# Kernel tuning notes

Hardware: AMD Instinct MI355X
Metric: run time of the kernel (lower is better)

## Reference

```python
import jax, jax.numpy as jnp
import numpy as np

B, N = 32, 2048

def _gather(pts, idx):
    # pts: [B,N,C], idx: [B,...] int -> [B,...,C]
    b = pts.shape[0]
    flat = jnp.take_along_axis(pts, idx.reshape(b, -1)[:, :, None], axis=1)
    return flat.reshape(idx.shape + (pts.shape[-1],))

def _fps(xyz, npoint):
    # iterative farthest point sampling, start at index 0
    b, n, _ = xyz.shape
    def step(carry, _):
        dist, far = carry
        centroid = _gather(xyz, far[:, None])            # [B,1,3]
        d = jnp.sum((xyz - centroid) ** 2, axis=-1)      # [B,N]
        dist = jnp.minimum(dist, d)
        nxt = jnp.argmax(dist, axis=-1).astype(jnp.int32)
        return (dist, nxt), far
    init = (jnp.full((b, n), 1e10, xyz.dtype), jnp.zeros((b,), jnp.int32))
    _, idxs = jax.lax.scan(step, init, None, length=npoint)
    return jnp.transpose(idxs)                           # [B,npoint]

def _ball_query(radius, nsample, xyz, new_xyz):
    n = xyz.shape[1]
    sqr = jnp.sum((new_xyz[:, :, None, :] - xyz[:, None, :, :]) ** 2, axis=-1)  # [B,S,N]
    idx = jnp.broadcast_to(jnp.arange(n, dtype=jnp.int32), sqr.shape)
    idx = jnp.where(sqr > radius * radius, n, idx)
    idx = jnp.sort(idx, axis=-1)[:, :, :nsample]
    first = idx[:, :, :1]
    return jnp.where(idx == n, first, idx)               # [B,S,K]

def _mlp_max(x, params):
    # shared per-point MLP (1x1 conv) + max-pool over neighbors (BN at init == identity)
    for W, b in params:
        x = jax.nn.relu(jnp.einsum('bskc,dc->bskd', x, W) + b)
    return jnp.max(x, axis=2)                            # [B,S,out]

def _sa(xyz, points, npoint, radius, nsample, params):
    fidx = _fps(xyz, npoint)
    new_xyz = _gather(xyz, fidx)                         # [B,S,3]
    gidx = _ball_query(radius, nsample, xyz, new_xyz)
    grouped = _gather(xyz, gidx) - new_xyz[:, :, None, :]
    if points is not None:
        grouped = jnp.concatenate([grouped, _gather(points, gidx)], axis=-1)
    return new_xyz, _mlp_max(grouped, params)

def _sa_all(xyz, points, params):
    grouped = jnp.concatenate([xyz, points], axis=-1)[:, None]  # [B,1,N,C+3]
    return _mlp_max(grouped, params)[:, 0]               # [B,out]

def _linear(x, W, b):
    return x @ W.T + b

def _forward(points, grasp_pose, init_pose, final_pose, surfaces,
             sa1_w0, sa1_b0, sa1_w1, sa1_b1, sa1_w2, sa1_b2,
             sa2_w0, sa2_b0, sa2_w1, sa2_b1, sa2_w2, sa2_b2,
             emb_init, emb_final,
             pe_w0, pe_b0, pe_w1, pe_b1, pe_w2, pe_b2,
             fu_w0, fu_b0, fu_w1, fu_b1,
             os_w, os_b, oc_w, oc_b):
    sa1 = [(sa1_w0, sa1_b0), (sa1_w1, sa1_b1), (sa1_w2, sa1_b2)]
    sa2 = [(sa2_w0, sa2_b0), (sa2_w1, sa2_b1), (sa2_w2, sa2_b2)]
    l1_xyz, l1_points = _sa(points, None, 512, 0.2, 32, sa1)
    obj_feat = _sa_all(l1_xyz, l1_points, sa2)           # [B,256]
    ie = emb_init[surfaces[:, 0]]
    fe = emb_final[surfaces[:, 1]]
    x = jnp.concatenate([grasp_pose, init_pose, final_pose, ie, fe], axis=1)
    h = jax.nn.relu(_linear(x, pe_w0, pe_b0))
    h = jax.nn.relu(_linear(h, pe_w1, pe_b1))
    pose_feat = jax.nn.relu(_linear(h, pe_w2, pe_b2))
    fused = jnp.concatenate([obj_feat, pose_feat], axis=1)
    h = jax.nn.relu(_linear(fused, fu_w0, fu_b0))
    hidden = jax.nn.relu(_linear(h, fu_w1, fu_b1))
    return _linear(hidden, os_w, os_b), _linear(hidden, oc_w, oc_b)

def setup_inputs():
    key = jax.random.key(0)
    ks = jax.random.split(key, 24)
    def lin(k, o, i):
        return jax.random.normal(k, (o, i), jnp.float32) * (2.0 / i) ** 0.5
    z = lambda o: jnp.zeros((o,), jnp.float32)
    return {
        'points': jax.random.normal(ks[0], (B, N, 3), jnp.float32),
        'grasp_pose': jax.random.normal(ks[1], (B, 7), jnp.float32),
        'init_pose': jax.random.normal(ks[2], (B, 7), jnp.float32),
        'final_pose': jax.random.normal(ks[3], (B, 7), jnp.float32),
        'surfaces': jax.random.randint(ks[4], (B, 2), 0, 6),
        'sa1_w0': lin(ks[5], 64, 3), 'sa1_b0': z(64),
        'sa1_w1': lin(ks[6], 64, 64), 'sa1_b1': z(64),
        'sa1_w2': lin(ks[7], 128, 64), 'sa1_b2': z(128),
        'sa2_w0': lin(ks[8], 128, 131), 'sa2_b0': z(128),
        'sa2_w1': lin(ks[9], 128, 128), 'sa2_b1': z(128),
        'sa2_w2': lin(ks[10], 256, 128), 'sa2_b2': z(256),
        'emb_init': jax.random.normal(ks[11], (6, 8), jnp.float32),
        'emb_final': jax.random.normal(ks[12], (6, 8), jnp.float32),
        'pe_w0': lin(ks[13], 64, 37), 'pe_b0': z(64),
        'pe_w1': lin(ks[14], 128, 64), 'pe_b1': z(128),
        'pe_w2': lin(ks[15], 128, 128), 'pe_b2': z(128),
        'fu_w0': lin(ks[16], 128, 384), 'fu_b0': z(128),
        'fu_w1': lin(ks[17], 64, 128), 'fu_b1': z(64),
        'os_w': lin(ks[18], 1, 64), 'os_b': z(1),
        'oc_w': lin(ks[19], 1, 64), 'oc_b': z(1),
    }

def reference(points, grasp_pose, init_pose, final_pose, surfaces,
              sa1_w0, sa1_b0, sa1_w1, sa1_b1, sa1_w2, sa1_b2,
              sa2_w0, sa2_b0, sa2_w1, sa2_b1, sa2_w2, sa2_b2,
              emb_init, emb_final,
              pe_w0, pe_b0, pe_w1, pe_b1, pe_w2, pe_b2,
              fu_w0, fu_b0, fu_w1, fu_b1,
              os_w, os_b, oc_w, oc_b):
    return _forward(points, grasp_pose, init_pose, final_pose, surfaces,
                    sa1_w0, sa1_b0, sa1_w1, sa1_b1, sa1_w2, sa1_b2,
                    sa2_w0, sa2_b0, sa2_w1, sa2_b1, sa2_w2, sa2_b2,
                    emb_init, emb_final,
                    pe_w0, pe_b0, pe_w1, pe_b1, pe_w2, pe_b2,
                    fu_w0, fu_b0, fu_w1, fu_b1,
                    os_w, os_b, oc_w, oc_b)
```

## Files before the change

### kernel.cpp

```cpp
#include <hip/hip_runtime.h>

#define DEVINL __device__ __forceinline__

DEVINL float sq3(float ax, float ay, float az, float bx, float by, float bz) {
  float dx = __fsub_rn(ax, bx), dy = __fsub_rn(ay, by), dz = __fsub_rn(az, bz);
  return __fadd_rn(__fadd_rn(__fmul_rn(dx, dx), __fmul_rn(dy, dy)), __fmul_rn(dz, dz));
}

DEVINL float rdlane(float v, int l) {
  return __int_as_float(__builtin_amdgcn_readlane(__float_as_int(v), l));
}

template <int CTRL>
DEVINL float dpp_maxf(float v) {
  int o = __builtin_amdgcn_update_dpp(__float_as_int(v), __float_as_int(v),
                                      CTRL, 0xf, 0xf, false);
  return fmaxf(v, __int_as_float(o));
}
DEVINL float red32_maxf(float v) {
  v = dpp_maxf<0x111>(v); v = dpp_maxf<0x112>(v); v = dpp_maxf<0x114>(v);
  v = dpp_maxf<0x118>(v); v = dpp_maxf<0x142>(v);
  return v;
}
DEVINL float red64_maxf(float v) {
  v = red32_maxf(v); v = dpp_maxf<0x143>(v);
  return v;
}
template <int CTRL>
DEVINL unsigned long long dpp_maxk(unsigned long long k) {
  const unsigned lo = (unsigned)k, hi = (unsigned)(k >> 32);
  const unsigned olo = (unsigned)__builtin_amdgcn_update_dpp(
      (int)lo, (int)lo, CTRL, 0xf, 0xf, false);
  const unsigned ohi = (unsigned)__builtin_amdgcn_update_dpp(
      (int)hi, (int)hi, CTRL, 0xf, 0xf, false);
  const unsigned long long ok = ((unsigned long long)ohi << 32) | olo;
  return (ok > k) ? ok : k;
}
DEVINL unsigned long long red64_maxk(unsigned long long k) {
  k = dpp_maxk<0x111>(k); k = dpp_maxk<0x112>(k); k = dpp_maxk<0x114>(k);
  k = dpp_maxk<0x118>(k); k = dpp_maxk<0x142>(k); k = dpp_maxk<0x143>(k);
  return k;
}

__global__ __launch_bounds__(256) void k_wt(const float* __restrict__ w1,
                                            const float* __restrict__ w2,
                                            float* __restrict__ w1T,
                                            float* __restrict__ w2T) {
  const int i = blockIdx.x * 256 + threadIdx.x;
  if (i < 4096) {
    const int d = i >> 6, c = i & 63;
    w1T[c * 64 + d] = w1[i];
  }
  if (i < 8192) {
    const int e = i >> 6, c = i & 63;
    w2T[c * 128 + e] = w2[i];
  }
}

__global__ __launch_bounds__(256) void k_fps(const float* __restrict__ xyz,
                                             int* __restrict__ fidx) {
  const int b = blockIdx.x, t = threadIdx.x;
  __shared__ float xs[2048], ys[2048], zs[2048];
  __shared__ unsigned long long skey[2][4];
  __shared__ float4 scoord[2][4];
  const float* P = xyz + (size_t)b * 6144;
  for (int i = t; i < 2048; i += 256) {
    xs[i] = P[3 * i]; ys[i] = P[3 * i + 1]; zs[i] = P[3 * i + 2];
  }
  __syncthreads();
  float px[8], py[8], pz[8], dist[8];
#pragma unroll
  for (int j = 0; j < 8; ++j) {
    const int idx = j * 256 + t;
    px[j] = xs[idx]; py[j] = ys[idx]; pz[j] = zs[idx];
    dist[j] = 1e10f;
  }
  int far = 0;
  float cx = xs[0], cy = ys[0], cz = zs[0];
  int* out = fidx + b * 512;
  for (int it = 0; it < 512; ++it) {
    if (t == 0) out[it] = far;
    float bv = -1.0f;
    int bi = 0;
#pragma unroll
    for (int j = 0; j < 8; ++j) {
      const float d = sq3(px[j], py[j], pz[j], cx, cy, cz);
      const float nd = fminf(dist[j], d);
      dist[j] = nd;
      if (nd > bv) { bv = nd; bi = j * 256 + t; }
    }
    unsigned long long key =
        ((unsigned long long)__float_as_uint(bv) << 32) | (unsigned)(2047 - bi);
    key = red64_maxk(key);
    const int par = it & 1;
    if ((t & 63) == 63) {
      const int widx = 2047 - (int)((unsigned)key & 2047u);
      skey[par][t >> 6] = key;
      scoord[par][t >> 6] = make_float4(xs[widx], ys[widx], zs[widx], 0.0f);
    }
    __syncthreads();
    unsigned long long k0 = skey[par][0], k1 = skey[par][1];
    unsigned long long k2 = skey[par][2], k3 = skey[par][3];
    float4 c0 = scoord[par][0], c1 = scoord[par][1];
    float4 c2 = scoord[par][2], c3 = scoord[par][3];
    if (k1 > k0) { k0 = k1; c0 = c1; }
    if (k3 > k2) { k2 = k3; c2 = c3; }
    if (k2 > k0) { k0 = k2; c0 = c2; }
    far = 2047 - (int)((unsigned)k0 & 2047u);
    cx = c0.x; cy = c0.y; cz = c0.z;
  }
}

__global__ __launch_bounds__(256) void k_ballq(const float* __restrict__ xyz,
                                               const int* __restrict__ fidx,
                                               float* __restrict__ new_xyz,
                                               int* __restrict__ gidx,
                                               int* __restrict__ gn) {
  const int gw = (blockIdx.x * 256 + threadIdx.x) >> 6;
  const int lane = threadIdx.x & 63;
  const int b = gw >> 9;
  const float* P = xyz + (size_t)b * 6144;
  const int cidx = fidx[gw];
  const float cx = P[3 * cidx], cy = P[3 * cidx + 1], cz = P[3 * cidx + 2];
  if (lane < 3) new_xyz[(size_t)gw * 3 + lane] = P[3 * cidx + lane];
  int* g = gidx + (size_t)gw * 32;
  int base = 0;
  for (int c0 = 0; c0 < 2048; c0 += 64) {
    const int idx = c0 + lane;
    const float d = sq3(cx, cy, cz, P[3 * idx], P[3 * idx + 1], P[3 * idx + 2]);
    const bool in = !(d > 0.04f);
    const unsigned long long m = __ballot(in);
    if (in) {
      const int pos = base + (int)__popcll(m & ((1ull << lane) - 1ull));
      if (pos < 32) g[pos] = idx;
    }
    base += (int)__popcll(m);
    if (base >= 32) break;
  }
  if (lane == 0) gn[gw] = (base < 32) ? base : 32;
}

__global__ __launch_bounds__(256, 2) void k_sa1g(
    const float* __restrict__ xyz, const float* __restrict__ new_xyz,
    const int* __restrict__ gidx, const int* __restrict__ gn,
    const float* __restrict__ w0, const float* __restrict__ b0,
    const float* __restrict__ w1T, const float* __restrict__ b1,
    const float* __restrict__ w2T, const float* __restrict__ b2,
    float* __restrict__ l1p) {
  const int wv = threadIdx.x >> 6, lane = threadIdx.x & 63;
  const int g0 = (blockIdx.x * 4 + wv) * 8;
  float w1r[64], w2ra[64], w2rb[64];
#pragma unroll
  for (int c = 0; c < 64; ++c) w1r[c] = w1T[c * 64 + lane];
#pragma unroll
  for (int c = 0; c < 64; ++c) w2ra[c] = w2T[c * 128 + lane];
#pragma unroll
  for (int c = 0; c < 64; ++c) w2rb[c] = w2T[c * 128 + 64 + lane];
  const float w0x = w0[3 * lane], w0y = w0[3 * lane + 1], w0z = w0[3 * lane + 2];
  const float b0l = b0[lane], b1l = b1[lane];
  const float b2a = b2[lane], b2b = b2[lane + 64];
  for (int gi = 0; gi < 8; ++gi) {
    const int g = g0 + gi;
    const int b = g >> 9;
    const float* P = xyz + (size_t)b * 6144;
    const float nx = new_xyz[(size_t)g * 3], ny = new_xyz[(size_t)g * 3 + 1],
                nz = new_xyz[(size_t)g * 3 + 2];
    const int n = gn[g];
    const int* items = gidx + (size_t)g * 32;
    float acca = 0.0f, accb = 0.0f;
    for (int i = 0; i < n; ++i) {
      const int src = items[i];
      const float x = P[3 * src] - nx, y = P[3 * src + 1] - ny,
                  z = P[3 * src + 2] - nz;
      const float h = fmaxf(0.0f, fmaf(w0x, x, fmaf(w0y, y, fmaf(w0z, z, b0l))));
      float s0 = 0.f, s1 = 0.f, s2 = 0.f, s3 = 0.f;
#pragma unroll
      for (int c = 0; c < 64; c += 4) {
        s0 = fmaf(w1r[c], rdlane(h, c), s0);
        s1 = fmaf(w1r[c + 1], rdlane(h, c + 1), s1);
        s2 = fmaf(w1r[c + 2], rdlane(h, c + 2), s2);
        s3 = fmaf(w1r[c + 3], rdlane(h, c + 3), s3);
      }
      const float sv = fmaxf(0.0f, b1l + ((s0 + s1) + (s2 + s3)));
      float a0 = 0.f, a1 = 0.f, a2 = 0.f, a3 = 0.f;
      float u0 = 0.f, u1 = 0.f, u2 = 0.f, u3 = 0.f;
#pragma unroll
      for (int c = 0; c < 64; c += 4) {
        const float v0 = rdlane(sv, c), v1 = rdlane(sv, c + 1);
        const float v2 = rdlane(sv, c + 2), v3 = rdlane(sv, c + 3);
        a0 = fmaf(w2ra[c], v0, a0);
        a1 = fmaf(w2ra[c + 1], v1, a1);
        a2 = fmaf(w2ra[c + 2], v2, a2);
        a3 = fmaf(w2ra[c + 3], v3, a3);
        u0 = fmaf(w2rb[c], v0, u0);
        u1 = fmaf(w2rb[c + 1], v1, u1);
        u2 = fmaf(w2rb[c + 2], v2, u2);
        u3 = fmaf(w2rb[c + 3], v3, u3);
      }
      acca = fmaxf(acca, fmaxf(0.0f, b2a + ((a0 + a1) + (a2 + a3))));
      accb = fmaxf(accb, fmaxf(0.0f, b2b + ((u0 + u1) + (u2 + u3))));
    }
    float* outg = l1p + (size_t)g * 128;
    outg[lane] = acca;
    outg[lane + 64] = accb;
  }
}

__global__ __launch_bounds__(256, 2) void k_sa2_l0(
    const float* __restrict__ new_xyz, const float* __restrict__ l1p,
    const float* __restrict__ w0, const float* __restrict__ b0,
    float4* __restrict__ h0t4) {
  const int pb = blockIdx.x >> 4, ds = blockIdx.x & 15;
  const int t = threadIdx.x;
  const int d0 = ds * 8;
  const int m = pb * 256 + t;
  const float ax = new_xyz[(size_t)m * 3], ay = new_xyz[(size_t)m * 3 + 1],
              az = new_xyz[(size_t)m * 3 + 2];
  float4 av[32];
  const float4* lp = (const float4*)(l1p + (size_t)m * 128);
#pragma unroll
  for (int i = 0; i < 32; ++i) av[i] = lp[i];
  for (int dq = 0; dq < 2; ++dq) {
    float o[4];
#pragma unroll
    for (int k = 0; k < 4; ++k) {
      const int dd = 4 * dq + k;
      const float* wr = w0 + (size_t)(d0 + dd) * 131;
      float s = fmaf(wr[0], ax, fmaf(wr[1], ay, fmaf(wr[2], az, b0[d0 + dd])));
      float s0 = 0.f, s1 = 0.f, s2 = 0.f, s3 = 0.f;
#pragma unroll
      for (int i = 0; i < 32; ++i) {
        s0 = fmaf(wr[3 + 4 * i], av[i].x, s0);
        s1 = fmaf(wr[4 + 4 * i], av[i].y, s1);
        s2 = fmaf(wr[5 + 4 * i], av[i].z, s2);
        s3 = fmaf(wr[6 + 4 * i], av[i].w, s3);
      }
      o[k] = fmaxf(0.0f, s + ((s0 + s1) + (s2 + s3)));
    }
    h0t4[(size_t)(ds * 2 + dq) * 16384 + m] =
        make_float4(o[0], o[1], o[2], o[3]);
  }
}

__global__ __launch_bounds__(256, 2) void k_sa2_l1(
    const float4* __restrict__ h0t4, const float* __restrict__ w1,
    const float* __restrict__ b1, float4* __restrict__ h1t4) {
  const int pb = blockIdx.x >> 4, ds = blockIdx.x & 15;
  const int t = threadIdx.x;
  const int d0 = ds * 8;
  const int m = pb * 256 + t;
  float4 a4[32];
#pragma unroll
  for (int i = 0; i < 32; ++i) a4[i] = h0t4[(size_t)i * 16384 + m];
  for (int dq = 0; dq < 2; ++dq) {
    float o[4];
#pragma unroll
    for (int k = 0; k < 4; ++k) {
      const int dd = 4 * dq + k;
      const float* wr = w1 + (size_t)(d0 + dd) * 128;
      float s0 = 0.f, s1 = 0.f, s2 = 0.f, s3 = 0.f;
#pragma unroll
      for (int i = 0; i < 32; ++i) {
        s0 = fmaf(wr[4 * i], a4[i].x, s0);
        s1 = fmaf(wr[4 * i + 1], a4[i].y, s1);
        s2 = fmaf(wr[4 * i + 2], a4[i].z, s2);
        s3 = fmaf(wr[4 * i + 3], a4[i].w, s3);
      }
      o[k] = fmaxf(0.0f, b1[d0 + dd] + ((s0 + s1) + (s2 + s3)));
    }
    h1t4[(size_t)(ds * 2 + dq) * 16384 + m] =
        make_float4(o[0], o[1], o[2], o[3]);
  }
}

__global__ __launch_bounds__(256, 2) void k_sa2_l2max(
    const float4* __restrict__ h1t4, const float* __restrict__ w2,
    const float* __restrict__ b2, float* __restrict__ pmax) {
  const int pb = blockIdx.x >> 5, ds = blockIdx.x & 31;
  const int t = threadIdx.x;
  const int d0 = ds * 8;
  const int m = pb * 256 + t;
  const int b = m >> 9;
  const int wc = ((pb << 2) + (t >> 6)) & 7;
  float4 a4[32];
#pragma unroll
  for (int i = 0; i < 32; ++i) a4[i] = h1t4[(size_t)i * 16384 + m];
  for (int dq = 0; dq < 2; ++dq) {
#pragma unroll
    for (int k = 0; k < 4; ++k) {
      const int dd = 4 * dq + k;
      const float* wr = w2 + (size_t)(d0 + dd) * 128;
      float s0 = 0.f, s1 = 0.f, s2 = 0.f, s3 = 0.f;
#pragma unroll
      for (int i = 0; i < 32; ++i) {
        s0 = fmaf(wr[4 * i], a4[i].x, s0);
        s1 = fmaf(wr[4 * i + 1], a4[i].y, s1);
        s2 = fmaf(wr[4 * i + 2], a4[i].z, s2);
        s3 = fmaf(wr[4 * i + 3], a4[i].w, s3);
      }
      float v = fmaxf(0.0f, b2[d0 + dd] + ((s0 + s1) + (s2 + s3)));
      v = red64_maxf(v);
      if ((t & 63) == 63) pmax[((size_t)(b << 3) + wc) * 256 + d0 + dd] = v;
    }
  }
}

__global__ __launch_bounds__(64) void k_head(
    const float* __restrict__ pmax, const float* __restrict__ grasp,
    const float* __restrict__ initp, const float* __restrict__ finalp,
    const int* __restrict__ surf, const float* __restrict__ embi,
    const float* __restrict__ embf, const float* __restrict__ pw0,
    const float* __restrict__ pb0, const float* __restrict__ pw1,
    const float* __restrict__ pb1, const float* __restrict__ pw2,
    const float* __restrict__ pb2, const float* __restrict__ fw0,
    const float* __restrict__ fb0, const float* __restrict__ fw1,
    const float* __restrict__ fb1, const float* __restrict__ osw,
    const float* __restrict__ osb, const float* __restrict__ ocw,
    const float* __restrict__ ocb, float* __restrict__ out) {
  __shared__ float obj[256], xb[37], A0[64], A1[128], A2[128], F0[128], HID[64];
  const int b = blockIdx.x, l = threadIdx.x;
  const float* pm = pmax + (size_t)b * 2048;
  for (int e = l; e < 256; e += 64) {
    float v = pm[e];
#pragma unroll
    for (int w = 1; w < 8; ++w) v = fmaxf(v, pm[w * 256 + e]);
    obj[e] = v;
  }
  if (l < 7) xb[l] = grasp[b * 7 + l];
  else if (l < 14) xb[l] = initp[b * 7 + l - 7];
  else if (l < 21) xb[l] = finalp[b * 7 + l - 14];
  else if (l < 29) xb[l] = embi[surf[b * 2] * 8 + l - 21];
  else if (l < 37) xb[l] = embf[surf[b * 2 + 1] * 8 + l - 29];
  __syncthreads();
  {
    float s = pb0[l];
    const float* wr = pw0 + l * 37;
#pragma unroll
    for (int c = 0; c < 37; ++c) s = fmaf(xb[c], wr[c], s);
    A0[l] = fmaxf(0.f, s);
  }
  __syncthreads();
#pragma unroll
  for (int dd = 0; dd < 2; ++dd) {
    const int d = l + dd * 64;
    float s = pb1[d];
    const float* wr = pw1 + d * 64;
#pragma unroll
    for (int c = 0; c < 64; ++c) s = fmaf(A0[c], wr[c], s);
    A1[d] = fmaxf(0.f, s);
  }
  __syncthreads();
#pragma unroll
  for (int dd = 0; dd < 2; ++dd) {
    const int d = l + dd * 64;
    float s = pb2[d];
    const float* wr = pw2 + d * 128;
#pragma unroll 16
    for (int c = 0; c < 128; ++c) s = fmaf(A1[c], wr[c], s);
    A2[d] = fmaxf(0.f, s);
  }
  __syncthreads();
#pragma unroll
  for (int dd = 0; dd < 2; ++dd) {
    const int d = l + dd * 64;
    float s = fb0[d];
    const float* wr = fw0 + d * 384;
#pragma unroll 16
    for (int c = 0; c < 256; ++c) s = fmaf(obj[c], wr[c], s);
#pragma unroll 16
    for (int c = 0; c < 128; ++c) s = fmaf(A2[c], wr[256 + c], s);
    F0[d] = fmaxf(0.f, s);
  }
  __syncthreads();
  {
    float s = fb1[l];
    const float* wr = fw1 + l * 128;
#pragma unroll 16
    for (int c = 0; c < 128; ++c) s = fmaf(F0[c], wr[c], s);
    HID[l] = fmaxf(0.f, s);
  }
  __syncthreads();
  float v1 = HID[l] * osw[l];
  float v2 = HID[l] * ocw[l];
#pragma unroll
  for (int off = 1; off < 64; off <<= 1) {
    v1 += __shfl_xor(v1, off);
    v2 += __shfl_xor(v2, off);
  }
  if (l == 0) {
    out[b] = v1 + osb[0];
    out[32 + b] = v2 + ocb[0];
  }
}

extern "C" void kernel_launch(void* const* d_in, const int* in_sizes, int n_in,
                              void* d_out, int out_size, void* d_ws, size_t ws_size,
                              hipStream_t stream) {
  const float* points  = (const float*)d_in[0];
  const float* grasp   = (const float*)d_in[1];
  const float* initp   = (const float*)d_in[2];
  const float* finalp  = (const float*)d_in[3];
  const int*   surf    = (const int*)d_in[4];
  const float* sa1_w0  = (const float*)d_in[5];
  const float* sa1_b0  = (const float*)d_in[6];
  const float* sa1_w1  = (const float*)d_in[7];
  const float* sa1_b1  = (const float*)d_in[8];
  const float* sa1_w2  = (const float*)d_in[9];
  const float* sa1_b2  = (const float*)d_in[10];
  const float* sa2_w0  = (const float*)d_in[11];
  const float* sa2_b0  = (const float*)d_in[12];
  const float* sa2_w1  = (const float*)d_in[13];
  const float* sa2_b1  = (const float*)d_in[14];
  const float* sa2_w2  = (const float*)d_in[15];
  const float* sa2_b2  = (const float*)d_in[16];
  const float* embi    = (const float*)d_in[17];
  const float* embf    = (const float*)d_in[18];
  const float* pe_w0   = (const float*)d_in[19];
  const float* pe_b0   = (const float*)d_in[20];
  const float* pe_w1   = (const float*)d_in[21];
  const float* pe_b1   = (const float*)d_in[22];
  const float* pe_w2   = (const float*)d_in[23];
  const float* pe_b2   = (const float*)d_in[24];
  const float* fu_w0   = (const float*)d_in[25];
  const float* fu_b0   = (const float*)d_in[26];
  const float* fu_w1   = (const float*)d_in[27];
  const float* fu_b1   = (const float*)d_in[28];
  const float* os_w    = (const float*)d_in[29];
  const float* os_b    = (const float*)d_in[30];
  const float* oc_w    = (const float*)d_in[31];
  const float* oc_b    = (const float*)d_in[32];

  char* ws = (char*)d_ws;
  int*    fidx    = (int*)(ws + 0);
  float*  new_xyz = (float*)(ws + 65536);
  int*    gidx    = (int*)(ws + 262144);
  float*  l1p     = (float*)(ws + 2359296);
  float4* h0t4    = (float4*)(ws + 10747904);
  float*  pmax    = (float*)(ws + 19136512);
  int*    gn      = (int*)(ws + 19398656);
  float*  w1T     = (float*)(ws + 19464192);
  float*  w2T     = (float*)(ws + 19480576);
  float4* h1t4    = (float4*)l1p;

  float* out = (float*)d_out;

  k_wt<<<32, 256, 0, stream>>>(sa1_w1, sa1_w2, w1T, w2T);
  k_fps<<<32, 256, 0, stream>>>(points, fidx);
  k_ballq<<<4096, 256, 0, stream>>>(points, fidx, new_xyz, gidx, gn);
  k_sa1g<<<512, 256, 0, stream>>>(points, new_xyz, gidx, gn, sa1_w0, sa1_b0,
                                  w1T, sa1_b1, w2T, sa1_b2, l1p);
  k_sa2_l0<<<1024, 256, 0, stream>>>(new_xyz, l1p, sa2_w0, sa2_b0, h0t4);
  k_sa2_l1<<<1024, 256, 0, stream>>>(h0t4, sa2_w1, sa2_b1, h1t4);
  k_sa2_l2max<<<2048, 256, 0, stream>>>(h1t4, sa2_w2, sa2_b2, pmax);
  k_head<<<32, 64, 0, stream>>>(pmax, grasp, initp, finalp, surf, embi, embf,
                                pe_w0, pe_b0, pe_w1, pe_b1, pe_w2, pe_b2, fu_w0,
                                fu_b0, fu_w1, fu_b1, os_w, os_b, oc_w, oc_b, out);
}
```

Measured before the change: 411.3 us.

## Fuse FPS, ball query and SA1 MLP into one persistent ticketed kernel

Merges the farthest-point-sampling, ball-query and first set-abstraction MLP kernels into one persistent kernel of 128 blocks. The first 32 blocks run FPS and publish sampled indices to global memory in batches of 8. All waves, including the FPS blocks once they finish, then pull work items from an atomic ticket counter and spin-wait on a -1 sentinel until their index is published. This lets the grouping and MLP work overlap the long serial FPS loop and removes two launches plus the gidx/gn round-trip for the neighbour count. The trade-offs are that fewer waves do the MLP work than the old 512-block launch, and correctness now depends on cross-block spin-waiting plus two extra memsets.

```diff
diff --git a/kernel.cpp b/kernel.cpp
--- a/kernel.cpp
+++ b/kernel.cpp
@@ -17,13 +17,9 @@
                                       CTRL, 0xf, 0xf, false);
   return fmaxf(v, __int_as_float(o));
 }
-DEVINL float red32_maxf(float v) {
+DEVINL float red64_maxf(float v) {
   v = dpp_maxf<0x111>(v); v = dpp_maxf<0x112>(v); v = dpp_maxf<0x114>(v);
-  v = dpp_maxf<0x118>(v); v = dpp_maxf<0x142>(v);
-  return v;
-}
-DEVINL float red64_maxf(float v) {
-  v = red32_maxf(v); v = dpp_maxf<0x143>(v);
+  v = dpp_maxf<0x118>(v); v = dpp_maxf<0x142>(v); v = dpp_maxf<0x143>(v);
   return v;
 }
 template <int CTRL>
@@ -57,98 +53,79 @@
   }
 }
 
-__global__ __launch_bounds__(256) void k_fps(const float* __restrict__ xyz,
-                                             int* __restrict__ fidx) {
-  const int b = blockIdx.x, t = threadIdx.x;
+__global__ __launch_bounds__(256, 2) void k_mega(
+    const float* __restrict__ xyz, int* __restrict__ fidx,
+    unsigned* __restrict__ ticket, float* __restrict__ new_xyz,
+    int* __restrict__ gidx, const float* __restrict__ w0,
+    const float* __restrict__ b0, const float* __restrict__ w1T,
+    const float* __restrict__ b1, const float* __restrict__ w2T,
+    const float* __restrict__ b2, float* __restrict__ l1p) {
   __shared__ float xs[2048], ys[2048], zs[2048];
   __shared__ unsigned long long skey[2][4];
   __shared__ float4 scoord[2][4];
-  const float* P = xyz + (size_t)b * 6144;
-  for (int i = t; i < 2048; i += 256) {
-    xs[i] = P[3 * i]; ys[i] = P[3 * i + 1]; zs[i] = P[3 * i + 2];
-  }
-  __syncthreads();
-  float px[8], py[8], pz[8], dist[8];
-#pragma unroll
-  for (int j = 0; j < 8; ++j) {
-    const int idx = j * 256 + t;
-    px[j] = xs[idx]; py[j] = ys[idx]; pz[j] = zs[idx];
-    dist[j] = 1e10f;
-  }
-  int far = 0;
-  float cx = xs[0], cy = ys[0], cz = zs[0];
-  int* out = fidx + b * 512;
-  for (int it = 0; it < 512; ++it) {
-    if (t == 0) out[it] = far;
-    float bv = -1.0f;
-    int bi = 0;
+  __shared__ int out_lds[512];
+  const int t = threadIdx.x;
+
+  if (blockIdx.x < 32) {
+    const int b = blockIdx.x;
+    const float* P = xyz + (size_t)b * 6144;
+    for (int i = t; i < 2048; i += 256) {
+      xs[i] = P[3 * i]; ys[i] = P[3 * i + 1]; zs[i] = P[3 * i + 2];
+    }
+    __syncthreads();
+    float px[8], py[8], pz[8], dist[8];
 #pragma unroll
     for (int j = 0; j < 8; ++j) {
-      const float d = sq3(px[j], py[j], pz[j], cx, cy, cz);
-      const float nd = fminf(dist[j], d);
-      dist[j] = nd;
-      if (nd > bv) { bv = nd; bi = j * 256 + t; }
-    }
-    unsigned long long key =
-        ((unsigned long long)__float_as_uint(bv) << 32) | (unsigned)(2047 - bi);
-    key = red64_maxk(key);
-    const int par = it & 1;
-    if ((t & 63) == 63) {
-      const int widx = 2047 - (int)((unsigned)key & 2047u);
-      skey[par][t >> 6] = key;
-      scoord[par][t >> 6] = make_float4(xs[widx], ys[widx], zs[widx], 0.0f);
-    }
-    __syncthreads();
-    unsigned long long k0 = skey[par][0], k1 = skey[par][1];
-    unsigned long long k2 = skey[par][2], k3 = skey[par][3];
-    float4 c0 = scoord[par][0], c1 = scoord[par][1];
-    float4 c2 = scoord[par][2], c3 = scoord[par][3];
-    if (k1 > k0) { k0 = k1; c0 = c1; }
-    if (k3 > k2) { k2 = k3; c2 = c3; }
-    if (k2 > k0) { k0 = k2; c0 = c2; }
-    far = 2047 - (int)((unsigned)k0 & 2047u);
-    cx = c0.x; cy = c0.y; cz = c0.z;
-  }
-}
-
-__global__ __launch_bounds__(256) void k_ballq(const float* __restrict__ xyz,
-                                               const int* __restrict__ fidx,
-                                               float* __restrict__ new_xyz,
-                                               int* __restrict__ gidx,
-                                               int* __restrict__ gn) {
-  const int gw = (blockIdx.x * 256 + threadIdx.x) >> 6;
-  const int lane = threadIdx.x & 63;
-  const int b = gw >> 9;
-  const float* P = xyz + (size_t)b * 6144;
-  const int cidx = fidx[gw];
-  const float cx = P[3 * cidx], cy = P[3 * cidx + 1], cz = P[3 * cidx + 2];
-  if (lane < 3) new_xyz[(size_t)gw * 3 + lane] = P[3 * cidx + lane];
-  int* g = gidx + (size_t)gw * 32;
-  int base = 0;
-  for (int c0 = 0; c0 < 2048; c0 += 64) {
-    const int idx = c0 + lane;
-    const float d = sq3(cx, cy, cz, P[3 * idx], P[3 * idx + 1], P[3 * idx + 2]);
-    const bool in = !(d > 0.04f);
-    const unsigned long long m = __ballot(in);
-    if (in) {
-      const int pos = base + (int)__popcll(m & ((1ull << lane) - 1ull));
-      if (pos < 32) g[pos] = idx;
-    }
-    base += (int)__popcll(m);
-    if (base >= 32) break;
-  }
-  if (lane == 0) gn[gw] = (base < 32) ? base : 32;
-}
-
-__global__ __launch_bounds__(256, 2) void k_sa1g(
-    const float* __restrict__ xyz, const float* __restrict__ new_xyz,
-    const int* __restrict__ gidx, const int* __restrict__ gn,
-    const float* __restrict__ w0, const float* __restrict__ b0,
-    const float* __restrict__ w1T, const float* __restrict__ b1,
-    const float* __restrict__ w2T, const float* __restrict__ b2,
-    float* __restrict__ l1p) {
-  const int wv = threadIdx.x >> 6, lane = threadIdx.x & 63;
-  const int g0 = (blockIdx.x * 4 + wv) * 8;
+      const int idx = j * 256 + t;
+      px[j] = xs[idx]; py[j] = ys[idx]; pz[j] = zs[idx];
+      dist[j] = 1e10f;
+    }
+    int far = 0;
+    float cx = xs[0], cy = ys[0], cz = zs[0];
+    int* outg = fidx + b * 512;
+    for (int it = 0; it < 512; ++it) {
+      if (t == 0) out_lds[it] = far;
+      if ((it & 7) == 0 && it != 0 && t < 8) {
+        const int idx = it - 8 + t;
+        __hip_atomic_store(&outg[idx], out_lds[idx], __ATOMIC_RELAXED,
+                           __HIP_MEMORY_SCOPE_AGENT);
+      }
+      float bv = -1.0f;
+      int bi = 0;
+#pragma unroll
+      for (int j = 0; j < 8; ++j) {
+        const float d = sq3(px[j], py[j], pz[j], cx, cy, cz);
+        const float nd = fminf(dist[j], d);
+        dist[j] = nd;
+        if (nd > bv) { bv = nd; bi = j * 256 + t; }
+      }
+      unsigned long long key =
+          ((unsigned long long)__float_as_uint(bv) << 32) |
+          (unsigned)(2047 - bi);
+      key = red64_maxk(key);
+      const int par = it & 1;
+      if ((t & 63) == 63) {
+        const int widx = 2047 - (int)((unsigned)key & 2047u);
+        skey[par][t >> 6] = key;
+        scoord[par][t >> 6] = make_float4(xs[widx], ys[widx], zs[widx], 0.0f);
+      }
+      __syncthreads();
+      unsigned long long k0 = skey[par][0], k1 = skey[par][1];
+      unsigned long long k2 = skey[par][2], k3 = skey[par][3];
+      float4 c0 = scoord[par][0], c1 = scoord[par][1];
+      float4 c2 = scoord[par][2], c3 = scoord[par][3];
+      if (k1 > k0) { k0 = k1; c0 = c1; }
+      if (k3 > k2) { k2 = k3; c2 = c3; }
+      if (k2 > k0) { k0 = k2; c0 = c2; }
+      far = 2047 - (int)((unsigned)k0 & 2047u);
+      cx = c0.x; cy = c0.y; cz = c0.z;
+    }
+    if (t < 8)
+      __hip_atomic_store(&outg[504 + t], out_lds[504 + t], __ATOMIC_RELAXED,
+                         __HIP_MEMORY_SCOPE_AGENT);
+  }
+
+  const int lane = t & 63;
   float w1r[64], w2ra[64], w2rb[64];
 #pragma unroll
   for (int c = 0; c < 64; ++c) w1r[c] = w1T[c * 64 + lane];
@@ -156,23 +133,47 @@
   for (int c = 0; c < 64; ++c) w2ra[c] = w2T[c * 128 + lane];
 #pragma unroll
   for (int c = 0; c < 64; ++c) w2rb[c] = w2T[c * 128 + 64 + lane];
-  const float w0x = w0[3 * lane], w0y = w0[3 * lane + 1], w0z = w0[3 * lane + 2];
+  const float w0x = w0[3 * lane], w0y = w0[3 * lane + 1],
+              w0z = w0[3 * lane + 2];
   const float b0l = b0[lane], b1l = b1[lane];
   const float b2a = b2[lane], b2b = b2[lane + 64];
-  for (int gi = 0; gi < 8; ++gi) {
-    const int g = g0 + gi;
-    const int b = g >> 9;
-    const float* P = xyz + (size_t)b * 6144;
-    const float nx = new_xyz[(size_t)g * 3], ny = new_xyz[(size_t)g * 3 + 1],
-                nz = new_xyz[(size_t)g * 3 + 2];
-    const int n = gn[g];
-    const int* items = gidx + (size_t)g * 32;
+  for (;;) {
+    unsigned tk = 0;
+    if (lane == 0) tk = atomicAdd(ticket, 1u);
+    tk = (unsigned)__builtin_amdgcn_readfirstlane((int)tk);
+    if (tk >= 16384u) break;
+    const int s = (int)(tk >> 5), bb = (int)(tk & 31);
+    const int g = bb * 512 + s;
+    int cidx;
+    while ((cidx = __hip_atomic_load(&fidx[bb * 512 + s], __ATOMIC_RELAXED,
+                                     __HIP_MEMORY_SCOPE_AGENT)) < 0)
+      __builtin_amdgcn_s_sleep(16);
+    const float* P = xyz + (size_t)bb * 6144;
+    const float cx = P[3 * cidx], cy = P[3 * cidx + 1], cz = P[3 * cidx + 2];
+    if (lane < 3) new_xyz[(size_t)g * 3 + lane] = P[3 * cidx + lane];
+    int* gq = gidx + (size_t)g * 32;
+    int base = 0;
+    for (int c0 = 0; c0 < 2048; c0 += 64) {
+      const int idx = c0 + lane;
+      const float d =
+          sq3(cx, cy, cz, P[3 * idx], P[3 * idx + 1], P[3 * idx + 2]);
+      const bool in = !(d > 0.04f);
+      const unsigned long long m = __ballot(in);
+      if (in) {
+        const int pos = base + (int)__popcll(m & ((1ull << lane) - 1ull));
+        if (pos < 32) gq[pos] = idx;
+      }
+      base += (int)__popcll(m);
+      if (base >= 32) break;
+    }
+    const int n = (base < 32) ? base : 32;
     float acca = 0.0f, accb = 0.0f;
     for (int i = 0; i < n; ++i) {
-      const int src = items[i];
-      const float x = P[3 * src] - nx, y = P[3 * src + 1] - ny,
-                  z = P[3 * src + 2] - nz;
-      const float h = fmaxf(0.0f, fmaf(w0x, x, fmaf(w0y, y, fmaf(w0z, z, b0l))));
+      const int src = gq[i];
+      const float x = P[3 * src] - cx, y = P[3 * src + 1] - cy,
+                  z = P[3 * src + 2] - cz;
+      const float h =
+          fmaxf(0.0f, fmaf(w0x, x, fmaf(w0y, y, fmaf(w0z, z, b0l))));
       float s0 = 0.f, s1 = 0.f, s2 = 0.f, s3 = 0.f;
 #pragma unroll
       for (int c = 0; c < 64; c += 4) {
@@ -200,9 +201,9 @@
       acca = fmaxf(acca, fmaxf(0.0f, b2a + ((a0 + a1) + (a2 + a3))));
       accb = fmaxf(accb, fmaxf(0.0f, b2b + ((u0 + u1) + (u2 + u3))));
     }
-    float* outg = l1p + (size_t)g * 128;
-    outg[lane] = acca;
-    outg[lane + 64] = accb;
+    float* outl = l1p + (size_t)g * 128;
+    outl[lane] = acca;
+    outl[lane + 64] = accb;
   }
 }
 
@@ -431,24 +432,25 @@
   const float* oc_b    = (const float*)d_in[32];
 
   char* ws = (char*)d_ws;
-  int*    fidx    = (int*)(ws + 0);
-  float*  new_xyz = (float*)(ws + 65536);
-  int*    gidx    = (int*)(ws + 262144);
-  float*  l1p     = (float*)(ws + 2359296);
-  float4* h0t4    = (float4*)(ws + 10747904);
-  float*  pmax    = (float*)(ws + 19136512);
-  int*    gn      = (int*)(ws + 19398656);
-  float*  w1T     = (float*)(ws + 19464192);
-  float*  w2T     = (float*)(ws + 19480576);
-  float4* h1t4    = (float4*)l1p;
+  int*      fidx    = (int*)(ws + 0);
+  float*    new_xyz = (float*)(ws + 65536);
+  int*      gidx    = (int*)(ws + 262144);
+  float*    l1p     = (float*)(ws + 2359296);
+  float4*   h0t4    = (float4*)(ws + 10747904);
+  float*    pmax    = (float*)(ws + 19136512);
+  unsigned* ticket  = (unsigned*)(ws + 19398656);
+  float*    w1T     = (float*)(ws + 19398720);
+  float*    w2T     = (float*)(ws + 19415104);
+  float4*   h1t4    = (float4*)l1p;
 
   float* out = (float*)d_out;
 
+  hipMemsetAsync(fidx, 0xFF, 65536, stream);
+  hipMemsetAsync(ticket, 0, 64, stream);
+
   k_wt<<<32, 256, 0, stream>>>(sa1_w1, sa1_w2, w1T, w2T);
-  k_fps<<<32, 256, 0, stream>>>(points, fidx);
-  k_ballq<<<4096, 256, 0, stream>>>(points, fidx, new_xyz, gidx, gn);
-  k_sa1g<<<512, 256, 0, stream>>>(points, new_xyz, gidx, gn, sa1_w0, sa1_b0,
-                                  w1T, sa1_b1, w2T, sa1_b2, l1p);
+  k_mega<<<128, 256, 0, stream>>>(points, fidx, ticket, new_xyz, gidx, sa1_w0,
+                                  sa1_b0, w1T, sa1_b1, w2T, sa1_b2, l1p);
   k_sa2_l0<<<1024, 256, 0, stream>>>(new_xyz, l1p, sa2_w0, sa2_b0, h0t4);
   k_sa2_l1<<<1024, 256, 0, stream>>>(h0t4, sa2_w1, sa2_b1, h1t4);
   k_sa2_l2max<<<2048, 256, 0, stream>>>(h1t4, sa2_w2, sa2_b2, pmax);
```

Measured after the change: 443.1 us. +7.7%, slower.

## Fuse ball query into SA1 group MLP and weight transpose into FPS

Applied to the files above, without the earlier changes.

The weight-transpose kernel is folded into the FPS launch as 32 extra blocks. The ball-query kernel is merged into the SA1 grouping/MLP kernel, with each wave now computing its own neighbour list into shared memory. This removes two launches and the global round-trip of gidx/gn. The cost is that the neighbour search now runs serially inside the register-heavy MLP kernel at 2 blocks per CU rather than in its own wide launch.

```diff
diff --git a/kernel.cpp b/kernel.cpp
--- a/kernel.cpp
+++ b/kernel.cpp
@@ -17,13 +17,9 @@
                                       CTRL, 0xf, 0xf, false);
   return fmaxf(v, __int_as_float(o));
 }
-DEVINL float red32_maxf(float v) {
+DEVINL float red64_maxf(float v) {
   v = dpp_maxf<0x111>(v); v = dpp_maxf<0x112>(v); v = dpp_maxf<0x114>(v);
-  v = dpp_maxf<0x118>(v); v = dpp_maxf<0x142>(v);
-  return v;
-}
-DEVINL float red64_maxf(float v) {
-  v = red32_maxf(v); v = dpp_maxf<0x143>(v);
+  v = dpp_maxf<0x118>(v); v = dpp_maxf<0x142>(v); v = dpp_maxf<0x143>(v);
   return v;
 }
 template <int CTRL>
@@ -42,23 +38,20 @@
   return k;
 }
 
-__global__ __launch_bounds__(256) void k_wt(const float* __restrict__ w1,
-                                            const float* __restrict__ w2,
-                                            float* __restrict__ w1T,
-                                            float* __restrict__ w2T) {
-  const int i = blockIdx.x * 256 + threadIdx.x;
-  if (i < 4096) {
-    const int d = i >> 6, c = i & 63;
-    w1T[c * 64 + d] = w1[i];
-  }
-  if (i < 8192) {
+__global__ __launch_bounds__(256) void k_fps_wt(
+    const float* __restrict__ xyz, int* __restrict__ fidx,
+    const float* __restrict__ w1, const float* __restrict__ w2,
+    float* __restrict__ w1T, float* __restrict__ w2T) {
+  if (blockIdx.x >= 32) {
+    const int i = (blockIdx.x - 32) * 256 + threadIdx.x;
+    if (i < 4096) {
+      const int d = i >> 6, c = i & 63;
+      w1T[c * 64 + d] = w1[i];
+    }
     const int e = i >> 6, c = i & 63;
     w2T[c * 128 + e] = w2[i];
-  }
-}
-
-__global__ __launch_bounds__(256) void k_fps(const float* __restrict__ xyz,
-                                             int* __restrict__ fidx) {
+    return;
+  }
   const int b = blockIdx.x, t = threadIdx.x;
   __shared__ float xs[2048], ys[2048], zs[2048];
   __shared__ unsigned long long skey[2][4];
@@ -111,42 +104,13 @@
   }
 }
 
-__global__ __launch_bounds__(256) void k_ballq(const float* __restrict__ xyz,
-                                               const int* __restrict__ fidx,
-                                               float* __restrict__ new_xyz,
-                                               int* __restrict__ gidx,
-                                               int* __restrict__ gn) {
-  const int gw = (blockIdx.x * 256 + threadIdx.x) >> 6;
-  const int lane = threadIdx.x & 63;
-  const int b = gw >> 9;
-  const float* P = xyz + (size_t)b * 6144;
-  const int cidx = fidx[gw];
-  const float cx = P[3 * cidx], cy = P[3 * cidx + 1], cz = P[3 * cidx + 2];
-  if (lane < 3) new_xyz[(size_t)gw * 3 + lane] = P[3 * cidx + lane];
-  int* g = gidx + (size_t)gw * 32;
-  int base = 0;
-  for (int c0 = 0; c0 < 2048; c0 += 64) {
-    const int idx = c0 + lane;
-    const float d = sq3(cx, cy, cz, P[3 * idx], P[3 * idx + 1], P[3 * idx + 2]);
-    const bool in = !(d > 0.04f);
-    const unsigned long long m = __ballot(in);
-    if (in) {
-      const int pos = base + (int)__popcll(m & ((1ull << lane) - 1ull));
-      if (pos < 32) g[pos] = idx;
-    }
-    base += (int)__popcll(m);
-    if (base >= 32) break;
-  }
-  if (lane == 0) gn[gw] = (base < 32) ? base : 32;
-}
-
-__global__ __launch_bounds__(256, 2) void k_sa1g(
-    const float* __restrict__ xyz, const float* __restrict__ new_xyz,
-    const int* __restrict__ gidx, const int* __restrict__ gn,
-    const float* __restrict__ w0, const float* __restrict__ b0,
-    const float* __restrict__ w1T, const float* __restrict__ b1,
-    const float* __restrict__ w2T, const float* __restrict__ b2,
-    float* __restrict__ l1p) {
+__global__ __launch_bounds__(256, 2) void k_bsa1(
+    const float* __restrict__ xyz, const int* __restrict__ fidx,
+    float* __restrict__ new_xyz, const float* __restrict__ w0,
+    const float* __restrict__ b0, const float* __restrict__ w1T,
+    const float* __restrict__ b1, const float* __restrict__ w2T,
+    const float* __restrict__ b2, float* __restrict__ l1p) {
+  __shared__ int sgq[4][32];
   const int wv = threadIdx.x >> 6, lane = threadIdx.x & 63;
   const int g0 = (blockIdx.x * 4 + wv) * 8;
   float w1r[64], w2ra[64], w2rb[64];
@@ -161,18 +125,33 @@
   const float b2a = b2[lane], b2b = b2[lane + 64];
   for (int gi = 0; gi < 8; ++gi) {
     const int g = g0 + gi;
-    const int b = g >> 9;
-    const float* P = xyz + (size_t)b * 6144;
-    const float nx = new_xyz[(size_t)g * 3], ny = new_xyz[(size_t)g * 3 + 1],
-                nz = new_xyz[(size_t)g * 3 + 2];
-    const int n = gn[g];
-    const int* items = gidx + (size_t)g * 32;
+    const int bb = g >> 9;
+    const float* P = xyz + (size_t)bb * 6144;
+    const int cidx = fidx[g];
+    const float cx = P[3 * cidx], cy = P[3 * cidx + 1], cz = P[3 * cidx + 2];
+    if (lane < 3) new_xyz[(size_t)g * 3 + lane] = P[3 * cidx + lane];
+    int base = 0;
+    for (int c0 = 0; c0 < 2048; c0 += 64) {
+      const int idx = c0 + lane;
+      const float d =
+          sq3(cx, cy, cz, P[3 * idx], P[3 * idx + 1], P[3 * idx + 2]);
+      const bool in = !(d > 0.04f);
+      const unsigned long long m = __ballot(in);
+      if (in) {
+        const int pos = base + (int)__popcll(m & ((1ull << lane) - 1ull));
+        if (pos < 32) sgq[wv][pos] = idx;
+      }
+      base += (int)__popcll(m);
+      if (base >= 32) break;
+    }
+    const int n = (base < 32) ? base : 32;
     float acca = 0.0f, accb = 0.0f;
     for (int i = 0; i < n; ++i) {
-      const int src = items[i];
-      const float x = P[3 * src] - nx, y = P[3 * src + 1] - ny,
-                  z = P[3 * src + 2] - nz;
-      const float h = fmaxf(0.0f, fmaf(w0x, x, fmaf(w0y, y, fmaf(w0z, z, b0l))));
+      const int src = sgq[wv][i];
+      const float x = P[3 * src] - cx, y = P[3 * src + 1] - cy,
+                  z = P[3 * src + 2] - cz;
+      const float h =
+          fmaxf(0.0f, fmaf(w0x, x, fmaf(w0y, y, fmaf(w0z, z, b0l))));
       float s0 = 0.f, s1 = 0.f, s2 = 0.f, s3 = 0.f;
 #pragma unroll
       for (int c = 0; c < 64; c += 4) {
@@ -433,22 +412,18 @@
   char* ws = (char*)d_ws;
   int*    fidx    = (int*)(ws + 0);
   float*  new_xyz = (float*)(ws + 65536);
-  int*    gidx    = (int*)(ws + 262144);
   float*  l1p     = (float*)(ws + 2359296);
   float4* h0t4    = (float4*)(ws + 10747904);
   float*  pmax    = (float*)(ws + 19136512);
-  int*    gn      = (int*)(ws + 19398656);
-  float*  w1T     = (float*)(ws + 19464192);
-  float*  w2T     = (float*)(ws + 19480576);
+  float*  w1T     = (float*)(ws + 19398720);
+  float*  w2T     = (float*)(ws + 19415104);
   float4* h1t4    = (float4*)l1p;
 
   float* out = (float*)d_out;
 
-  k_wt<<<32, 256, 0, stream>>>(sa1_w1, sa1_w2, w1T, w2T);
-  k_fps<<<32, 256, 0, stream>>>(points, fidx);
-  k_ballq<<<4096, 256, 0, stream>>>(points, fidx, new_xyz, gidx, gn);
-  k_sa1g<<<512, 256, 0, stream>>>(points, new_xyz, gidx, gn, sa1_w0, sa1_b0,
-                                  w1T, sa1_b1, w2T, sa1_b2, l1p);
+  k_fps_wt<<<64, 256, 0, stream>>>(points, fidx, sa1_w1, sa1_w2, w1T, w2T);
+  k_bsa1<<<512, 256, 0, stream>>>(points, fidx, new_xyz, sa1_w0, sa1_b0, w1T,
+                                  sa1_b1, w2T, sa1_b2, l1p);
   k_sa2_l0<<<1024, 256, 0, stream>>>(new_xyz, l1p, sa2_w0, sa2_b0, h0t4);
   k_sa2_l1<<<1024, 256, 0, stream>>>(h0t4, sa2_w1, sa2_b1, h1t4);
   k_sa2_l2max<<<2048, 256, 0, stream>>>(h1t4, sa2_w2, sa2_b2, pmax);
```

Result: slower. 435.3 us (+5.8%).
